# Performance work log

Hardware: AMD Instinct MI355X
Metric: run time of the kernel (lower is better)

The kernel has to match this reference:

```python
import jax, jax.numpy as jnp
import numpy as np

FEATURE_DIM = 512
NUM_HEADS = 8
HEAD_DIM = FEATURE_DIM // NUM_HEADS
B, L = 4, 2048


def setup_inputs() -> dict:
    key = jax.random.key(0)
    ks = jax.random.split(key, 10)
    s = 1.0 / np.sqrt(FEATURE_DIM)
    inp = {
        "ppg": jax.random.normal(ks[0], (B, FEATURE_DIM, L), dtype=jnp.float32),
        "ecg": jax.random.normal(ks[1], (B, FEATURE_DIM, L), dtype=jnp.float32),
        "Wq": jax.random.uniform(ks[2], (FEATURE_DIM, FEATURE_DIM), jnp.float32, -s, s),
        "bq": jnp.zeros((FEATURE_DIM,), jnp.float32),
        "Wk": jax.random.uniform(ks[3], (FEATURE_DIM, FEATURE_DIM), jnp.float32, -s, s),
        "bk": jnp.zeros((FEATURE_DIM,), jnp.float32),
        "Wv": jax.random.uniform(ks[4], (FEATURE_DIM, FEATURE_DIM), jnp.float32, -s, s),
        "bv": jnp.zeros((FEATURE_DIM,), jnp.float32),
        "Wo": jax.random.uniform(ks[5], (FEATURE_DIM, FEATURE_DIM), jnp.float32, -s, s),
        "bo": jnp.zeros((FEATURE_DIM,), jnp.float32),
    }
    return inp


def reference(ppg, ecg, Wq, bq, Wk, bk, Wv, bv, Wo, bo):
    # ppg/ecg: (B, C, L) -> (B, L, C)
    x = jnp.transpose(ppg, (0, 2, 1))
    y = jnp.transpose(ecg, (0, 2, 1))
    q = x @ Wq.T + bq  # (B, L, C)
    k = y @ Wk.T + bk
    v = y @ Wv.T + bv
    # split heads: (B, H, L, D)
    def split(t):
        return jnp.transpose(t.reshape(B, L, NUM_HEADS, HEAD_DIM), (0, 2, 1, 3))
    qh, kh, vh = split(q), split(k), split(v)
    scores = jnp.einsum('bhqd,bhkd->bhqk', qh, kh) / jnp.sqrt(jnp.float32(HEAD_DIM))
    probs = jax.nn.softmax(scores, axis=-1)  # dropout is identity in eval mode
    ctx = jnp.einsum('bhqk,bhkd->bhqd', probs, vh)
    ctx = jnp.transpose(ctx, (0, 2, 1, 3)).reshape(B, L, FEATURE_DIM)
    out = ctx @ Wo.T + bo + x  # residual with transposed ppg
    return jnp.transpose(out, (0, 2, 1))  # (B, C, L)
```

## Files before the change

### kernel.cpp

```cpp
#include <hip/hip_runtime.h>
#include <hip/hip_bf16.h>

static constexpr int Bc = 4;
static constexpr int Lc = 2048;
static constexpr int Cc = 512;
static constexpr int Hc = 8;
static constexpr int Dc = 64;

using short8  = __attribute__((ext_vector_type(8))) short;
using float4v = __attribute__((ext_vector_type(4))) float;

static __device__ __forceinline__ unsigned short f2bf(float f) {
    __hip_bfloat16 h = __float2bfloat16(f);
    return *reinterpret_cast<unsigned short*>(&h);
}

__global__ __launch_bounds__(256) void prep_kernel(
    const float* __restrict__ ppg, const float* __restrict__ ecg,
    const float* __restrict__ Wq, const float* __restrict__ Wk,
    const float* __restrict__ Wv, const float* __restrict__ Wo,
    unsigned short* __restrict__ Xt_ppg, unsigned short* __restrict__ Xt_ecg,
    unsigned short* __restrict__ Wbf)
{
    __shared__ float Ts[64 * 69];
    const int task = blockIdx.x;
    const int tid  = threadIdx.x;

    if (task < 2048) {
        const int src = task >> 10;
        const int rem = task & 1023;
        const int b   = rem >> 8;
        const int c0  = ((rem >> 5) & 7) * 64;
        const int l0  = (rem & 31) * 64;
        const float* X = src ? ecg : ppg;
        unsigned short* Xt = src ? Xt_ecg : Xt_ppg;

        #pragma unroll
        for (int j = 0; j < 4; ++j) {
            int idx = tid + j * 256;
            int c = idx >> 4, l4 = idx & 15;
            float4 v = *(const float4*)(X + ((size_t)b * Cc + c0 + c) * Lc + l0 + l4 * 4);
            Ts[c * 69 + l4 * 4 + 0] = v.x;
            Ts[c * 69 + l4 * 4 + 1] = v.y;
            Ts[c * 69 + l4 * 4 + 2] = v.z;
            Ts[c * 69 + l4 * 4 + 3] = v.w;
        }
        __syncthreads();
        #pragma unroll
        for (int j = 0; j < 8; ++j) {
            int u = tid + j * 256;
            int l = u >> 5, p2 = u & 31;
            float a = Ts[(2 * p2) * 69 + l];
            float bb = Ts[(2 * p2 + 1) * 69 + l];
            ushort2 pk; pk.x = f2bf(a); pk.y = f2bf(bb);
            *(ushort2*)(Xt + ((size_t)b * Lc + l0 + l) * Cc + c0 + 2 * p2) = pk;
        }
    } else {
        const int wb   = task - 2048;
        const int widx = wb >> 7;
        const float* W = widx == 0 ? Wq : widx == 1 ? Wk : widx == 2 ? Wv : Wo;
        size_t off = (size_t)(wb & 127) * 2048 + (size_t)tid * 8;
        float4 v0 = *(const float4*)(W + off);
        float4 v1 = *(const float4*)(W + off + 4);
        unsigned short pk[8] = {f2bf(v0.x), f2bf(v0.y), f2bf(v0.z), f2bf(v0.w),
                                f2bf(v1.x), f2bf(v1.y), f2bf(v1.z), f2bf(v1.w)};
        *(short8*)(Wbf + (size_t)widx * Cc * Cc + off) = *(const short8*)pk;
    }
}

__global__ __launch_bounds__(256) void proj_kernel(
    const unsigned short* __restrict__ Xt_ppg,
    const unsigned short* __restrict__ Xt_ecg,
    const unsigned short* __restrict__ Wbf,
    const float* __restrict__ bq, const float* __restrict__ bk,
    const float* __restrict__ bv,
    unsigned short* __restrict__ Qw, unsigned short* __restrict__ Kw,
    unsigned short* __restrict__ Vtw)
{
    constexpr int LDW = 72;
    const int z = blockIdx.z, p = z >> 2, b = z & 3;
    const int l0 = blockIdx.x * 128, n0 = blockIdx.y * 128;
    const unsigned short* X = (p == 0) ? Xt_ppg : Xt_ecg;
    const unsigned short* W = Wbf + (size_t)p * Cc * Cc;
    const float* bias = (p == 0) ? bq : (p == 1) ? bk : bv;

    const int tid = threadIdx.x, wave = tid >> 6, lane = tid & 63;
    const int l16 = lane & 15, quad = lane >> 4;
    const int wr = wave >> 1, wc = wave & 1;

    __shared__ __align__(16) unsigned short At[128 * LDW];
    __shared__ __align__(16) unsigned short Bt[128 * LDW];

    float4v acc[4][4] = {};
    short8 areg[4], breg[4];

    const int srow = tid >> 3, sc8 = tid & 7;
    #pragma unroll
    for (int j = 0; j < 4; ++j) {
        areg[j] = *(const short8*)(X + ((size_t)b * Lc + l0 + srow + j * 32) * Cc + sc8 * 8);
        breg[j] = *(const short8*)(W + (size_t)(n0 + srow + j * 32) * Cc + sc8 * 8);
    }

    for (int c0 = 0; c0 < Cc; c0 += 64) {
        #pragma unroll
        for (int j = 0; j < 4; ++j) {
            *(short8*)&At[(srow + j * 32) * LDW + sc8 * 8] = areg[j];
            *(short8*)&Bt[(srow + j * 32) * LDW + sc8 * 8] = breg[j];
        }
        __syncthreads();

        if (c0 + 64 < Cc) {
            #pragma unroll
            for (int j = 0; j < 4; ++j) {
                areg[j] = *(const short8*)(X + ((size_t)b * Lc + l0 + srow + j * 32) * Cc
                                           + c0 + 64 + sc8 * 8);
                breg[j] = *(const short8*)(W + (size_t)(n0 + srow + j * 32) * Cc
                                           + c0 + 64 + sc8 * 8);
            }
        }

        const unsigned short* Am = (p < 2) ? At : Bt;
        const unsigned short* Bm = (p < 2) ? Bt : At;

        #pragma unroll
        for (int ks = 0; ks < 2; ++ks) {
            short8 bf[4];
            #pragma unroll
            for (int nt = 0; nt < 4; ++nt)
                bf[nt] = *(const short8*)&Bm[(wc * 64 + nt * 16 + l16) * LDW
                                             + ks * 32 + quad * 8];
            #pragma unroll
            for (int mt = 0; mt < 4; ++mt) {
                short8 af = *(const short8*)&Am[(wr * 64 + mt * 16 + l16) * LDW
                                                + ks * 32 + quad * 8];
                #pragma unroll
                for (int nt = 0; nt < 4; ++nt)
                    acc[mt][nt] = __builtin_amdgcn_mfma_f32_16x16x32_bf16(
                        af, bf[nt], acc[mt][nt], 0, 0, 0);
            }
        }
        __syncthreads();
    }

    if (p < 2) {
        const float sc = (p == 0) ? 0.18033688011112042f : 1.0f;
        unsigned short* dst = (p == 0) ? Qw : Kw;
        #pragma unroll
        for (int nt = 0; nt < 4; ++nt) {
            int n = n0 + wc * 64 + nt * 16 + l16;
            int h = n >> 6, d = n & 63;
            int bh = b * Hc + h;
            float bia = bias[n];
            #pragma unroll
            for (int mt = 0; mt < 4; ++mt) {
                #pragma unroll
                for (int r = 0; r < 4; ++r) {
                    int l = l0 + wr * 64 + mt * 16 + quad * 4 + r;
                    dst[((size_t)bh * Lc + l) * Dc + d] =
                        f2bf((acc[mt][nt][r] + bia) * sc);
                }
            }
        }
    } else {
        #pragma unroll
        for (int mt = 0; mt < 4; ++mt) {
            #pragma unroll
            for (int r = 0; r < 4; ++r) {
                int n = n0 + wr * 64 + mt * 16 + quad * 4 + r;
                int h = n >> 6, d = n & 63;
                int bh = b * Hc + h;
                float bia = bias[n];
                #pragma unroll
                for (int nt = 0; nt < 4; ++nt) {
                    int l = l0 + wc * 64 + nt * 16 + l16;
                    Vtw[((size_t)bh * Dc + d) * Lc + l] = f2bf(acc[mt][nt][r] + bia);
                }
            }
        }
    }
}

__global__ __launch_bounds__(256, 4) void attn_mfma_kernel(
    const unsigned short* __restrict__ Qg,
    const unsigned short* __restrict__ Kg,
    const unsigned short* __restrict__ Vtg,
    float* __restrict__ O0, float* __restrict__ O1,
    float* __restrict__ lpart)
{
    constexpr int LDW = 72;
    const int bh    = blockIdx.y;
    const int split = blockIdx.z;
    const int q0    = blockIdx.x * 128;
    const int tid   = threadIdx.x;
    const int wave  = tid >> 6;
    const int lane  = tid & 63;
    const int l16   = lane & 15;
    const int quad  = lane >> 4;

    __shared__ __align__(16) unsigned short Kt[64 * LDW];
    __shared__ __align__(16) unsigned short Vt[64 * LDW];
    __shared__ __align__(16) unsigned short PT[128 * LDW];

    const int srow = tid >> 3, sc8 = tid & 7;

    const unsigned short* Qb = Qg + ((size_t)bh * Lc + q0) * Dc;
    #pragma unroll
    for (int j = 0; j < 4; ++j)
        *(short8*)&PT[(srow + j * 32) * LDW + sc8 * 8] =
            *(const short8*)(Qb + (srow + j * 32) * Dc + sc8 * 8);
    __syncthreads();

    short8 qf[2][2];
    #pragma unroll
    for (int qt = 0; qt < 2; ++qt)
        #pragma unroll
        for (int ks = 0; ks < 2; ++ks)
            qf[qt][ks] = *(const short8*)&PT[(wave * 32 + qt * 16 + l16) * LDW
                                             + ks * 32 + quad * 8];

    float4v O[2][4] = {};
    float lsum[2] = {0.0f, 0.0f};

    const unsigned short* Kb0 = Kg + (size_t)bh * Lc * Dc;
    const unsigned short* Vb0 = Vtg + (size_t)bh * (Dc * Lc);
    const int kbase = split * (Lc / 2);

    short8 kreg[2], vreg[2];
    #pragma unroll
    for (int j = 0; j < 2; ++j) {
        kreg[j] = *(const short8*)(Kb0 + (size_t)(kbase + srow + j * 32) * Dc + sc8 * 8);
        vreg[j] = *(const short8*)(Vb0 + (size_t)(srow + j * 32) * Lc + kbase + sc8 * 8);
    }

    for (int kc = kbase; kc < kbase + Lc / 2; kc += 64) {
        #pragma unroll
        for (int j = 0; j < 2; ++j) {
            *(short8*)&Kt[(srow + j * 32) * LDW + sc8 * 8] = kreg[j];
            *(short8*)&Vt[(srow + j * 32) * LDW + sc8 * 8] = vreg[j];
        }
        __syncthreads();

        if (kc + 64 < kbase + Lc / 2) {
            #pragma unroll
            for (int j = 0; j < 2; ++j) {
                kreg[j] = *(const short8*)(Kb0 + (size_t)(kc + 64 + srow + j * 32) * Dc
                                           + sc8 * 8);
                vreg[j] = *(const short8*)(Vb0 + (size_t)(srow + j * 32) * Lc
                                           + kc + 64 + sc8 * 8);
            }
        }

        float4v S[4][2];
        #pragma unroll
        for (int kt = 0; kt < 4; ++kt)
            #pragma unroll
            for (int qt = 0; qt < 2; ++qt)
                S[kt][qt] = (float4v){0.f, 0.f, 0.f, 0.f};
        #pragma unroll
        for (int ks = 0; ks < 2; ++ks) {
            #pragma unroll
            for (int kt = 0; kt < 4; ++kt) {
                short8 af = *(const short8*)&Kt[(kt * 16 + l16) * LDW
                                                + ks * 32 + quad * 8];
                #pragma unroll
                for (int qt = 0; qt < 2; ++qt)
                    S[kt][qt] = __builtin_amdgcn_mfma_f32_16x16x32_bf16(
                        af, qf[qt][ks], S[kt][qt], 0, 0, 0);
            }
        }

        #pragma unroll
        for (int qt = 0; qt < 2; ++qt) {
            #pragma unroll
            for (int kt = 0; kt < 4; ++kt) {
                float p0 = __builtin_amdgcn_exp2f(S[kt][qt][0]);
                float p1 = __builtin_amdgcn_exp2f(S[kt][qt][1]);
                float p2 = __builtin_amdgcn_exp2f(S[kt][qt][2]);
                float p3 = __builtin_amdgcn_exp2f(S[kt][qt][3]);
                lsum[qt] += (p0 + p1) + (p2 + p3);
                ushort4 pk;
                pk.x = f2bf(p0); pk.y = f2bf(p1); pk.z = f2bf(p2); pk.w = f2bf(p3);
                *(ushort4*)&PT[(wave * 32 + qt * 16 + l16) * LDW
                               + kt * 16 + quad * 4] = pk;
            }
        }

        #pragma unroll
        for (int ks = 0; ks < 2; ++ks) {
            short8 pf[2];
            #pragma unroll
            for (int qt = 0; qt < 2; ++qt)
                pf[qt] = *(const short8*)&PT[(wave * 32 + qt * 16 + l16) * LDW
                                             + ks * 32 + quad * 8];
            #pragma unroll
            for (int dt = 0; dt < 4; ++dt) {
                short8 vf = *(const short8*)&Vt[(dt * 16 + l16) * LDW
                                                + ks * 32 + quad * 8];
                #pragma unroll
                for (int qt = 0; qt < 2; ++qt)
                    O[qt][dt] = __builtin_amdgcn_mfma_f32_16x16x32_bf16(
                        pf[qt], vf, O[qt][dt], 0, 0, 0);
            }
        }
        __syncthreads();
    }

    const int b = bh >> 3, h = bh & 7;
    float* Op = split ? O1 : O0;
    float* lp = lpart + (size_t)split * (Bc * Hc) * Lc + (size_t)bh * Lc;

    #pragma unroll
    for (int qt = 0; qt < 2; ++qt) {
        float t = lsum[qt];
        t += __shfl_xor(t, 16, 64);
        t += __shfl_xor(t, 32, 64);
        if (quad == 0)
            lp[q0 + wave * 32 + qt * 16 + l16] = t;
        #pragma unroll
        for (int dt = 0; dt < 4; ++dt) {
            #pragma unroll
            for (int r = 0; r < 4; ++r) {
                int q = q0 + wave * 32 + qt * 16 + quad * 4 + r;
                Op[((size_t)b * Lc + q) * Cc + h * Dc + dt * 16 + l16] =
                    O[qt][dt][r];
            }
        }
    }
}

__global__ __launch_bounds__(256) void combine_kernel(
    const float* __restrict__ O0, const float* __restrict__ O1,
    const float* __restrict__ lpart, unsigned short* __restrict__ ctx)
{
    const int row = blockIdx.x;
    const int b   = row >> 11;
    const int l   = row & (Lc - 1);
    const int tid = threadIdx.x;
    const int c   = tid * 2;
    const int h   = c >> 6;

    const size_t lplane = (size_t)(Bc * Hc) * Lc;
    float denom = lpart[(size_t)(b * Hc + h) * Lc + l]
                + lpart[lplane + (size_t)(b * Hc + h) * Lc + l];
    float inv = 1.0f / denom;

    size_t off = (size_t)row * Cc + c;
    float2 a = *(const float2*)(O0 + off);
    float2 bb = *(const float2*)(O1 + off);
    ushort2 pk;
    pk.x = f2bf((a.x + bb.x) * inv);
    pk.y = f2bf((a.y + bb.y) * inv);
    *(ushort2*)(ctx + off) = pk;
}

__global__ __launch_bounds__(256) void outproj_kernel(
    const unsigned short* __restrict__ ctx, const unsigned short* __restrict__ Wo_bf,
    const float* __restrict__ bo, const float* __restrict__ ppg,
    float* __restrict__ out)
{
    constexpr int LDW = 72;
    const int b = blockIdx.z;
    const int l0 = blockIdx.x * 128, n0 = blockIdx.y * 64;
    const int tid = threadIdx.x, wave = tid >> 6, lane = tid & 63;
    const int l16 = lane & 15, quad = lane >> 4;

    __shared__ __align__(16) unsigned short At[64 * LDW];
    __shared__ __align__(16) unsigned short Bt[128 * LDW];

    float4v acc[4][2] = {};
    short8 areg[2], breg[4];

    const int srow = tid >> 3, sc8 = tid & 7;
    #pragma unroll
    for (int j = 0; j < 2; ++j)
        areg[j] = *(const short8*)(Wo_bf + (size_t)(n0 + srow + j * 32) * Cc + sc8 * 8);
    #pragma unroll
    for (int j = 0; j < 4; ++j)
        breg[j] = *(const short8*)(ctx + ((size_t)b * Lc + l0 + srow + j * 32) * Cc + sc8 * 8);

    for (int c0 = 0; c0 < Cc; c0 += 64) {
        #pragma unroll
        for (int j = 0; j < 2; ++j)
            *(short8*)&At[(srow + j * 32) * LDW + sc8 * 8] = areg[j];
        #pragma unroll
        for (int j = 0; j < 4; ++j)
            *(short8*)&Bt[(srow + j * 32) * LDW + sc8 * 8] = breg[j];
        __syncthreads();

        if (c0 + 64 < Cc) {
            #pragma unroll
            for (int j = 0; j < 2; ++j)
                areg[j] = *(const short8*)(Wo_bf + (size_t)(n0 + srow + j * 32) * Cc
                                           + c0 + 64 + sc8 * 8);
            #pragma unroll
            for (int j = 0; j < 4; ++j)
                breg[j] = *(const short8*)(ctx + ((size_t)b * Lc + l0 + srow + j * 32) * Cc
                                           + c0 + 64 + sc8 * 8);
        }

        #pragma unroll
        for (int ks = 0; ks < 2; ++ks) {
            short8 bf[2];
            #pragma unroll
            for (int nt = 0; nt < 2; ++nt)
                bf[nt] = *(const short8*)&Bt[(wave * 32 + nt * 16 + l16) * LDW
                                             + ks * 32 + quad * 8];
            #pragma unroll
            for (int mt = 0; mt < 4; ++mt) {
                short8 af = *(const short8*)&At[(mt * 16 + l16) * LDW
                                                + ks * 32 + quad * 8];
                #pragma unroll
                for (int nt = 0; nt < 2; ++nt)
                    acc[mt][nt] = __builtin_amdgcn_mfma_f32_16x16x32_bf16(
                        af, bf[nt], acc[mt][nt], 0, 0, 0);
            }
        }
        __syncthreads();
    }

    #pragma unroll
    for (int mt = 0; mt < 4; ++mt) {
        #pragma unroll
        for (int r = 0; r < 4; ++r) {
            int n = n0 + mt * 16 + quad * 4 + r;
            float bia = bo[n];
            #pragma unroll
            for (int nt = 0; nt < 2; ++nt) {
                int l = l0 + wave * 32 + nt * 16 + l16;
                size_t oidx = ((size_t)b * Cc + n) * Lc + l;
                out[oidx] = acc[mt][nt][r] + bia + ppg[oidx];
            }
        }
    }
}

extern "C" void kernel_launch(void* const* d_in, const int* in_sizes, int n_in,
                              void* d_out, int out_size, void* d_ws, size_t ws_size,
                              hipStream_t stream) {
    const float* ppg = (const float*)d_in[0];
    const float* ecg = (const float*)d_in[1];
    const float* Wq  = (const float*)d_in[2];
    const float* bq  = (const float*)d_in[3];
    const float* Wk  = (const float*)d_in[4];
    const float* bk  = (const float*)d_in[5];
    const float* Wv  = (const float*)d_in[6];
    const float* bv  = (const float*)d_in[7];
    const float* Wo  = (const float*)d_in[8];
    const float* bo  = (const float*)d_in[9];
    float* out = (float*)d_out;

    unsigned short* base   = (unsigned short*)d_ws;
    const size_t M = 1024 * 1024;
    unsigned short* Xt_ppg = base;
    unsigned short* Xt_ecg = base + 4 * M;
    unsigned short* Wbf    = base + 8 * M;
    unsigned short* Qw     = base + 9 * M;
    unsigned short* Kw     = base + 13 * M;
    unsigned short* Vtw    = base + 17 * M;
    float* Opart0 = (float*)base;
    float* Opart1 = (float*)(base + 21 * M);
    float* lpart  = (float*)(base + 29 * M);
    unsigned short* ctx = Qw;

    prep_kernel<<<2560, 256, 0, stream>>>(ppg, ecg, Wq, Wk, Wv, Wo,
                                          Xt_ppg, Xt_ecg, Wbf);

    dim3 g1(Lc / 128, Cc / 128, 3 * Bc);
    proj_kernel<<<g1, 256, 0, stream>>>(Xt_ppg, Xt_ecg, Wbf, bq, bk, bv,
                                        Qw, Kw, Vtw);

    dim3 g2(Lc / 128, Bc * Hc, 2);
    attn_mfma_kernel<<<g2, 256, 0, stream>>>(Qw, Kw, Vtw, Opart0, Opart1, lpart);

    combine_kernel<<<Bc * Lc, 256, 0, stream>>>(Opart0, Opart1, lpart, ctx);

    dim3 g3(Lc / 128, Cc / 64, Bc);
    outproj_kernel<<<g3, 256, 0, stream>>>(ctx, Wbf + (size_t)3 * Cc * Cc,
                                           bo, ppg, out);
}
```

Before: 184.7 us.

## Fuse split-K combine into attention via atomic counter, enlarge attention and outproj tiles

Removes the separate combine kernel: each attention block writes its partial output in bf16, bumps a per-tile atomic counter, and the second-arriving block reads the other partial plus both row sums to write the normalized ctx. The attention tile grows to 256 queries per block, which doubles K/V reuse at the cost of registers (launch bounds drop to 2 blocks per SM). The output projection tile grows to 128x128 with a 2x2 wave layout. This adds a memset, threadfences and bf16 rounding of the partial sums, and halves the attention grid to 256 blocks, which may underfill the device.

```diff
diff --git a/kernel.cpp b/kernel.cpp
--- a/kernel.cpp
+++ b/kernel.cpp
@@ -13,6 +13,9 @@
 static __device__ __forceinline__ unsigned short f2bf(float f) {
     __hip_bfloat16 h = __float2bfloat16(f);
     return *reinterpret_cast<unsigned short*>(&h);
+}
+static __device__ __forceinline__ float bf2f(unsigned short u) {
+    return __uint_as_float(((unsigned int)u) << 16);
 }
 
 __global__ __launch_bounds__(256) void prep_kernel(
@@ -180,17 +183,20 @@
     }
 }
 
-__global__ __launch_bounds__(256, 4) void attn_mfma_kernel(
+__global__ __launch_bounds__(256, 2) void attn_mfma_kernel(
     const unsigned short* __restrict__ Qg,
     const unsigned short* __restrict__ Kg,
     const unsigned short* __restrict__ Vtg,
-    float* __restrict__ O0, float* __restrict__ O1,
-    float* __restrict__ lpart)
+    unsigned short* __restrict__ Opart0,
+    unsigned short* __restrict__ Opart1,
+    float* __restrict__ lpart,
+    unsigned short* __restrict__ ctx,
+    int* __restrict__ ctr)
 {
     constexpr int LDW = 72;
     const int bh    = blockIdx.y;
     const int split = blockIdx.z;
-    const int q0    = blockIdx.x * 128;
+    const int q0    = blockIdx.x * 256;
     const int tid   = threadIdx.x;
     const int wave  = tid >> 6;
     const int lane  = tid & 63;
@@ -199,27 +205,28 @@
 
     __shared__ __align__(16) unsigned short Kt[64 * LDW];
     __shared__ __align__(16) unsigned short Vt[64 * LDW];
-    __shared__ __align__(16) unsigned short PT[128 * LDW];
+    __shared__ __align__(16) unsigned short PT[256 * LDW];
+    __shared__ int s_old;
 
     const int srow = tid >> 3, sc8 = tid & 7;
 
     const unsigned short* Qb = Qg + ((size_t)bh * Lc + q0) * Dc;
     #pragma unroll
-    for (int j = 0; j < 4; ++j)
+    for (int j = 0; j < 8; ++j)
         *(short8*)&PT[(srow + j * 32) * LDW + sc8 * 8] =
             *(const short8*)(Qb + (srow + j * 32) * Dc + sc8 * 8);
     __syncthreads();
 
-    short8 qf[2][2];
-    #pragma unroll
-    for (int qt = 0; qt < 2; ++qt)
+    short8 qf[4][2];
+    #pragma unroll
+    for (int qt = 0; qt < 4; ++qt)
         #pragma unroll
         for (int ks = 0; ks < 2; ++ks)
-            qf[qt][ks] = *(const short8*)&PT[(wave * 32 + qt * 16 + l16) * LDW
+            qf[qt][ks] = *(const short8*)&PT[(wave * 64 + qt * 16 + l16) * LDW
                                              + ks * 32 + quad * 8];
 
-    float4v O[2][4] = {};
-    float lsum[2] = {0.0f, 0.0f};
+    float4v O[4][4] = {};
+    float lsum[4] = {0.f, 0.f, 0.f, 0.f};
 
     const unsigned short* Kb0 = Kg + (size_t)bh * Lc * Dc;
     const unsigned short* Vb0 = Vtg + (size_t)bh * (Dc * Lc);
@@ -250,11 +257,11 @@
             }
         }
 
-        float4v S[4][2];
+        float4v S[4][4];
         #pragma unroll
         for (int kt = 0; kt < 4; ++kt)
             #pragma unroll
-            for (int qt = 0; qt < 2; ++qt)
+            for (int qt = 0; qt < 4; ++qt)
                 S[kt][qt] = (float4v){0.f, 0.f, 0.f, 0.f};
         #pragma unroll
         for (int ks = 0; ks < 2; ++ks) {
@@ -263,14 +270,14 @@
                 short8 af = *(const short8*)&Kt[(kt * 16 + l16) * LDW
                                                 + ks * 32 + quad * 8];
                 #pragma unroll
-                for (int qt = 0; qt < 2; ++qt)
+                for (int qt = 0; qt < 4; ++qt)
                     S[kt][qt] = __builtin_amdgcn_mfma_f32_16x16x32_bf16(
                         af, qf[qt][ks], S[kt][qt], 0, 0, 0);
             }
         }
 
         #pragma unroll
-        for (int qt = 0; qt < 2; ++qt) {
+        for (int qt = 0; qt < 4; ++qt) {
             #pragma unroll
             for (int kt = 0; kt < 4; ++kt) {
                 float p0 = __builtin_amdgcn_exp2f(S[kt][qt][0]);
@@ -280,24 +287,24 @@
                 lsum[qt] += (p0 + p1) + (p2 + p3);
                 ushort4 pk;
                 pk.x = f2bf(p0); pk.y = f2bf(p1); pk.z = f2bf(p2); pk.w = f2bf(p3);
-                *(ushort4*)&PT[(wave * 32 + qt * 16 + l16) * LDW
+                *(ushort4*)&PT[(wave * 64 + qt * 16 + l16) * LDW
                                + kt * 16 + quad * 4] = pk;
             }
         }
 
         #pragma unroll
         for (int ks = 0; ks < 2; ++ks) {
-            short8 pf[2];
-            #pragma unroll
-            for (int qt = 0; qt < 2; ++qt)
-                pf[qt] = *(const short8*)&PT[(wave * 32 + qt * 16 + l16) * LDW
+            short8 pf[4];
+            #pragma unroll
+            for (int qt = 0; qt < 4; ++qt)
+                pf[qt] = *(const short8*)&PT[(wave * 64 + qt * 16 + l16) * LDW
                                              + ks * 32 + quad * 8];
             #pragma unroll
             for (int dt = 0; dt < 4; ++dt) {
                 short8 vf = *(const short8*)&Vt[(dt * 16 + l16) * LDW
                                                 + ks * 32 + quad * 8];
                 #pragma unroll
-                for (int qt = 0; qt < 2; ++qt)
+                for (int qt = 0; qt < 4; ++qt)
                     O[qt][dt] = __builtin_amdgcn_mfma_f32_16x16x32_bf16(
                         pf[qt], vf, O[qt][dt], 0, 0, 0);
             }
@@ -306,51 +313,56 @@
     }
 
     const int b = bh >> 3, h = bh & 7;
-    float* Op = split ? O1 : O0;
+    unsigned short* Om = split ? Opart1 : Opart0;
     float* lp = lpart + (size_t)split * (Bc * Hc) * Lc + (size_t)bh * Lc;
 
     #pragma unroll
-    for (int qt = 0; qt < 2; ++qt) {
+    for (int qt = 0; qt < 4; ++qt) {
         float t = lsum[qt];
         t += __shfl_xor(t, 16, 64);
         t += __shfl_xor(t, 32, 64);
         if (quad == 0)
-            lp[q0 + wave * 32 + qt * 16 + l16] = t;
+            lp[q0 + wave * 64 + qt * 16 + l16] = t;
+    }
+    #pragma unroll
+    for (int qt = 0; qt < 4; ++qt) {
         #pragma unroll
         for (int dt = 0; dt < 4; ++dt) {
             #pragma unroll
             for (int r = 0; r < 4; ++r) {
-                int q = q0 + wave * 32 + qt * 16 + quad * 4 + r;
-                Op[((size_t)b * Lc + q) * Cc + h * Dc + dt * 16 + l16] =
-                    O[qt][dt][r];
-            }
-        }
-    }
-}
-
-__global__ __launch_bounds__(256) void combine_kernel(
-    const float* __restrict__ O0, const float* __restrict__ O1,
-    const float* __restrict__ lpart, unsigned short* __restrict__ ctx)
-{
-    const int row = blockIdx.x;
-    const int b   = row >> 11;
-    const int l   = row & (Lc - 1);
-    const int tid = threadIdx.x;
-    const int c   = tid * 2;
-    const int h   = c >> 6;
-
-    const size_t lplane = (size_t)(Bc * Hc) * Lc;
-    float denom = lpart[(size_t)(b * Hc + h) * Lc + l]
-                + lpart[lplane + (size_t)(b * Hc + h) * Lc + l];
-    float inv = 1.0f / denom;
-
-    size_t off = (size_t)row * Cc + c;
-    float2 a = *(const float2*)(O0 + off);
-    float2 bb = *(const float2*)(O1 + off);
-    ushort2 pk;
-    pk.x = f2bf((a.x + bb.x) * inv);
-    pk.y = f2bf((a.y + bb.y) * inv);
-    *(ushort2*)(ctx + off) = pk;
+                int q = q0 + wave * 64 + qt * 16 + quad * 4 + r;
+                Om[((size_t)b * Lc + q) * Cc + h * Dc + dt * 16 + l16] =
+                    f2bf(O[qt][dt][r]);
+            }
+        }
+    }
+
+    __threadfence();
+    __syncthreads();
+    if (tid == 0)
+        s_old = atomicAdd(&ctr[bh * 8 + blockIdx.x], 1);
+    __syncthreads();
+
+    if (s_old == 1) {
+        __threadfence();
+        const unsigned short* Oo = split ? Opart0 : Opart1;
+        const float* lp0 = lpart + (size_t)bh * Lc;
+        const float* lp1 = lpart + (size_t)(Bc * Hc) * Lc + (size_t)bh * Lc;
+        #pragma unroll
+        for (int qt = 0; qt < 4; ++qt) {
+            #pragma unroll
+            for (int r = 0; r < 4; ++r) {
+                int q = q0 + wave * 64 + qt * 16 + quad * 4 + r;
+                float inv = 1.0f / (lp0[q] + lp1[q]);
+                #pragma unroll
+                for (int dt = 0; dt < 4; ++dt) {
+                    size_t off = ((size_t)b * Lc + q) * Cc + h * Dc + dt * 16 + l16;
+                    float other = bf2f(Oo[off]);
+                    ctx[off] = f2bf((O[qt][dt][r] + other) * inv);
+                }
+            }
+        }
+    }
 }
 
 __global__ __launch_bounds__(256) void outproj_kernel(
@@ -360,57 +372,55 @@
 {
     constexpr int LDW = 72;
     const int b = blockIdx.z;
-    const int l0 = blockIdx.x * 128, n0 = blockIdx.y * 64;
+    const int l0 = blockIdx.x * 128, n0 = blockIdx.y * 128;
     const int tid = threadIdx.x, wave = tid >> 6, lane = tid & 63;
     const int l16 = lane & 15, quad = lane >> 4;
-
-    __shared__ __align__(16) unsigned short At[64 * LDW];
+    const int wr = wave >> 1, wc = wave & 1;
+
+    __shared__ __align__(16) unsigned short At[128 * LDW];
     __shared__ __align__(16) unsigned short Bt[128 * LDW];
 
-    float4v acc[4][2] = {};
-    short8 areg[2], breg[4];
+    float4v acc[4][4] = {};
+    short8 areg[4], breg[4];
 
     const int srow = tid >> 3, sc8 = tid & 7;
     #pragma unroll
-    for (int j = 0; j < 2; ++j)
+    for (int j = 0; j < 4; ++j) {
         areg[j] = *(const short8*)(Wo_bf + (size_t)(n0 + srow + j * 32) * Cc + sc8 * 8);
-    #pragma unroll
-    for (int j = 0; j < 4; ++j)
         breg[j] = *(const short8*)(ctx + ((size_t)b * Lc + l0 + srow + j * 32) * Cc + sc8 * 8);
+    }
 
     for (int c0 = 0; c0 < Cc; c0 += 64) {
         #pragma unroll
-        for (int j = 0; j < 2; ++j)
+        for (int j = 0; j < 4; ++j) {
             *(short8*)&At[(srow + j * 32) * LDW + sc8 * 8] = areg[j];
-        #pragma unroll
-        for (int j = 0; j < 4; ++j)
             *(short8*)&Bt[(srow + j * 32) * LDW + sc8 * 8] = breg[j];
+        }
         __syncthreads();
 
         if (c0 + 64 < Cc) {
             #pragma unroll
-            for (int j = 0; j < 2; ++j)
+            for (int j = 0; j < 4; ++j) {
                 areg[j] = *(const short8*)(Wo_bf + (size_t)(n0 + srow + j * 32) * Cc
                                            + c0 + 64 + sc8 * 8);
-            #pragma unroll
-            for (int j = 0; j < 4; ++j)
                 breg[j] = *(const short8*)(ctx + ((size_t)b * Lc + l0 + srow + j * 32) * Cc
                                            + c0 + 64 + sc8 * 8);
+            }
         }
 
         #pragma unroll
         for (int ks = 0; ks < 2; ++ks) {
-            short8 bf[2];
-            #pragma unroll
-            for (int nt = 0; nt < 2; ++nt)
-                bf[nt] = *(const short8*)&Bt[(wave * 32 + nt * 16 + l16) * LDW
+            short8 bf[4];
+            #pragma unroll
+            for (int nt = 0; nt < 4; ++nt)
+                bf[nt] = *(const short8*)&Bt[(wc * 64 + nt * 16 + l16) * LDW
                                              + ks * 32 + quad * 8];
             #pragma unroll
             for (int mt = 0; mt < 4; ++mt) {
-                short8 af = *(const short8*)&At[(mt * 16 + l16) * LDW
+                short8 af = *(const short8*)&At[(wr * 64 + mt * 16 + l16) * LDW
                                                 + ks * 32 + quad * 8];
                 #pragma unroll
-                for (int nt = 0; nt < 2; ++nt)
+                for (int nt = 0; nt < 4; ++nt)
                     acc[mt][nt] = __builtin_amdgcn_mfma_f32_16x16x32_bf16(
                         af, bf[nt], acc[mt][nt], 0, 0, 0);
             }
@@ -422,11 +432,11 @@
     for (int mt = 0; mt < 4; ++mt) {
         #pragma unroll
         for (int r = 0; r < 4; ++r) {
-            int n = n0 + mt * 16 + quad * 4 + r;
+            int n = n0 + wr * 64 + mt * 16 + quad * 4 + r;
             float bia = bo[n];
             #pragma unroll
-            for (int nt = 0; nt < 2; ++nt) {
-                int l = l0 + wave * 32 + nt * 16 + l16;
+            for (int nt = 0; nt < 4; ++nt) {
+                int l = l0 + wc * 64 + nt * 16 + l16;
                 size_t oidx = ((size_t)b * Cc + n) * Lc + l;
                 out[oidx] = acc[mt][nt][r] + bia + ppg[oidx];
             }
@@ -457,10 +467,13 @@
     unsigned short* Qw     = base + 9 * M;
     unsigned short* Kw     = base + 13 * M;
     unsigned short* Vtw    = base + 17 * M;
-    float* Opart0 = (float*)base;
-    float* Opart1 = (float*)(base + 21 * M);
-    float* lpart  = (float*)(base + 29 * M);
-    unsigned short* ctx = Qw;
+    unsigned short* ctx    = base + 21 * M;
+    float* lpart = (float*)(base + 25 * M);
+    int*   ctr   = (int*)(base + 25 * M + 262144);
+    unsigned short* Opart0 = base;
+    unsigned short* Opart1 = base + 4 * M;
+
+    hipMemsetAsync(ctr, 0, 32 * 8 * sizeof(int), stream);
 
     prep_kernel<<<2560, 256, 0, stream>>>(ppg, ecg, Wq, Wk, Wv, Wo,
                                           Xt_ppg, Xt_ecg, Wbf);
@@ -469,12 +482,11 @@
     proj_kernel<<<g1, 256, 0, stream>>>(Xt_ppg, Xt_ecg, Wbf, bq, bk, bv,
                                         Qw, Kw, Vtw);
 
-    dim3 g2(Lc / 128, Bc * Hc, 2);
-    attn_mfma_kernel<<<g2, 256, 0, stream>>>(Qw, Kw, Vtw, Opart0, Opart1, lpart);
-
-    combine_kernel<<<Bc * Lc, 256, 0, stream>>>(Opart0, Opart1, lpart, ctx);
-
-    dim3 g3(Lc / 128, Cc / 64, Bc);
+    dim3 g2(Lc / 256, Bc * Hc, 2);
+    attn_mfma_kernel<<<g2, 256, 0, stream>>>(Qw, Kw, Vtw, Opart0, Opart1,
+                                             lpart, ctx, ctr);
+
+    dim3 g3(Lc / 128, Cc / 128, Bc);
     outproj_kernel<<<g3, 256, 0, stream>>>(ctx, Wbf + (size_t)3 * Cc * Cc,
                                            bo, ppg, out);
 }
```

Measured after the change: 291.0 us. 57.5% more time.

## Fuse split-K attention combine into output projection with bf16 partials

Applied to the files above, without the earlier changes.

The attention kernel now writes its two split partial outputs as bf16 instead of fp32, and the separate combine kernel is removed. The output projection reads both partials and the row sums, normalizes and converts to bf16 while staging its tiles in shared memory. The output tile grows to 128x128 per block. This removes one launch and the fp32 partial round trip, but drops the register prefetch double-buffering in the out-projection, redoes the combine work once per n-block, and adds rounding error from the bf16 partials.

```diff
diff --git a/kernel.cpp b/kernel.cpp
--- a/kernel.cpp
+++ b/kernel.cpp
@@ -13,6 +13,9 @@
 static __device__ __forceinline__ unsigned short f2bf(float f) {
     __hip_bfloat16 h = __float2bfloat16(f);
     return *reinterpret_cast<unsigned short*>(&h);
+}
+static __device__ __forceinline__ float bf2f(unsigned short u) {
+    return __uint_as_float(((unsigned int)u) << 16);
 }
 
 __global__ __launch_bounds__(256) void prep_kernel(
@@ -184,7 +187,8 @@
     const unsigned short* __restrict__ Qg,
     const unsigned short* __restrict__ Kg,
     const unsigned short* __restrict__ Vtg,
-    float* __restrict__ O0, float* __restrict__ O1,
+    unsigned short* __restrict__ O0,
+    unsigned short* __restrict__ O1,
     float* __restrict__ lpart)
 {
     constexpr int LDW = 72;
@@ -306,7 +310,7 @@
     }
 
     const int b = bh >> 3, h = bh & 7;
-    float* Op = split ? O1 : O0;
+    unsigned short* Om = split ? O1 : O0;
     float* lp = lpart + (size_t)split * (Bc * Hc) * Lc + (size_t)bh * Lc;
 
     #pragma unroll
@@ -321,98 +325,75 @@
             #pragma unroll
             for (int r = 0; r < 4; ++r) {
                 int q = q0 + wave * 32 + qt * 16 + quad * 4 + r;
-                Op[((size_t)b * Lc + q) * Cc + h * Dc + dt * 16 + l16] =
-                    O[qt][dt][r];
-            }
-        }
-    }
-}
-
-__global__ __launch_bounds__(256) void combine_kernel(
-    const float* __restrict__ O0, const float* __restrict__ O1,
-    const float* __restrict__ lpart, unsigned short* __restrict__ ctx)
-{
-    const int row = blockIdx.x;
-    const int b   = row >> 11;
-    const int l   = row & (Lc - 1);
-    const int tid = threadIdx.x;
-    const int c   = tid * 2;
-    const int h   = c >> 6;
-
-    const size_t lplane = (size_t)(Bc * Hc) * Lc;
-    float denom = lpart[(size_t)(b * Hc + h) * Lc + l]
-                + lpart[lplane + (size_t)(b * Hc + h) * Lc + l];
-    float inv = 1.0f / denom;
-
-    size_t off = (size_t)row * Cc + c;
-    float2 a = *(const float2*)(O0 + off);
-    float2 bb = *(const float2*)(O1 + off);
-    ushort2 pk;
-    pk.x = f2bf((a.x + bb.x) * inv);
-    pk.y = f2bf((a.y + bb.y) * inv);
-    *(ushort2*)(ctx + off) = pk;
+                Om[((size_t)b * Lc + q) * Cc + h * Dc + dt * 16 + l16] =
+                    f2bf(O[qt][dt][r]);
+            }
+        }
+    }
 }
 
 __global__ __launch_bounds__(256) void outproj_kernel(
-    const unsigned short* __restrict__ ctx, const unsigned short* __restrict__ Wo_bf,
+    const unsigned short* __restrict__ O0, const unsigned short* __restrict__ O1,
+    const float* __restrict__ lpart,
+    const unsigned short* __restrict__ Wo_bf,
     const float* __restrict__ bo, const float* __restrict__ ppg,
     float* __restrict__ out)
 {
     constexpr int LDW = 72;
     const int b = blockIdx.z;
-    const int l0 = blockIdx.x * 128, n0 = blockIdx.y * 64;
+    const int l0 = blockIdx.x * 128, n0 = blockIdx.y * 128;
     const int tid = threadIdx.x, wave = tid >> 6, lane = tid & 63;
     const int l16 = lane & 15, quad = lane >> 4;
-
-    __shared__ __align__(16) unsigned short At[64 * LDW];
+    const int wr = wave >> 1, wc = wave & 1;
+
+    __shared__ __align__(16) unsigned short At[128 * LDW];
     __shared__ __align__(16) unsigned short Bt[128 * LDW];
 
-    float4v acc[4][2] = {};
-    short8 areg[2], breg[4];
-
+    float4v acc[4][4] = {};
     const int srow = tid >> 3, sc8 = tid & 7;
-    #pragma unroll
-    for (int j = 0; j < 2; ++j)
-        areg[j] = *(const short8*)(Wo_bf + (size_t)(n0 + srow + j * 32) * Cc + sc8 * 8);
-    #pragma unroll
-    for (int j = 0; j < 4; ++j)
-        breg[j] = *(const short8*)(ctx + ((size_t)b * Lc + l0 + srow + j * 32) * Cc + sc8 * 8);
+    const size_t lplane = (size_t)(Bc * Hc) * Lc;
 
     for (int c0 = 0; c0 < Cc; c0 += 64) {
-        #pragma unroll
-        for (int j = 0; j < 2; ++j)
-            *(short8*)&At[(srow + j * 32) * LDW + sc8 * 8] = areg[j];
-        #pragma unroll
-        for (int j = 0; j < 4; ++j)
-            *(short8*)&Bt[(srow + j * 32) * LDW + sc8 * 8] = breg[j];
-        __syncthreads();
-
-        if (c0 + 64 < Cc) {
-            #pragma unroll
-            for (int j = 0; j < 2; ++j)
-                areg[j] = *(const short8*)(Wo_bf + (size_t)(n0 + srow + j * 32) * Cc
-                                           + c0 + 64 + sc8 * 8);
-            #pragma unroll
-            for (int j = 0; j < 4; ++j)
-                breg[j] = *(const short8*)(ctx + ((size_t)b * Lc + l0 + srow + j * 32) * Cc
-                                           + c0 + 64 + sc8 * 8);
-        }
+        const int h = c0 >> 6;
+        const float* lp0 = lpart + (size_t)(b * Hc + h) * Lc;
+        const float* lp1 = lp0 + lplane;
+
+        #pragma unroll
+        for (int j = 0; j < 4; ++j) {
+            int row = srow + j * 32;
+            *(short8*)&At[row * LDW + sc8 * 8] =
+                *(const short8*)(Wo_bf + (size_t)(n0 + row) * Cc + c0 + sc8 * 8);
+            int l = l0 + row;
+            float inv = 1.0f / (lp0[l] + lp1[l]);
+            size_t off = ((size_t)b * Lc + l) * Cc + c0 + sc8 * 8;
+            short8 a8 = *(const short8*)(O0 + off);
+            short8 b8 = *(const short8*)(O1 + off);
+            unsigned short pk[8];
+            #pragma unroll
+            for (int e = 0; e < 8; ++e) {
+                unsigned short ua = ((const unsigned short*)&a8)[e];
+                unsigned short ub = ((const unsigned short*)&b8)[e];
+                pk[e] = f2bf((bf2f(ua) + bf2f(ub)) * inv);
+            }
+            *(short8*)&Bt[row * LDW + sc8 * 8] = *(const short8*)pk;
+        }
+        __syncthreads();
 
         #pragma unroll
         for (int ks = 0; ks < 2; ++ks) {
-            short8 bf[2];
-            #pragma unroll
-            for (int nt = 0; nt < 2; ++nt)
-                bf[nt] = *(const short8*)&Bt[(wave * 32 + nt * 16 + l16) * LDW
-                                             + ks * 32 + quad * 8];
+            short8 bfr[4];
+            #pragma unroll
+            for (int nt = 0; nt < 4; ++nt)
+                bfr[nt] = *(const short8*)&Bt[(wc * 64 + nt * 16 + l16) * LDW
+                                              + ks * 32 + quad * 8];
             #pragma unroll
             for (int mt = 0; mt < 4; ++mt) {
-                short8 af = *(const short8*)&At[(mt * 16 + l16) * LDW
+                short8 af = *(const short8*)&At[(wr * 64 + mt * 16 + l16) * LDW
                                                 + ks * 32 + quad * 8];
                 #pragma unroll
-                for (int nt = 0; nt < 2; ++nt)
+                for (int nt = 0; nt < 4; ++nt)
                     acc[mt][nt] = __builtin_amdgcn_mfma_f32_16x16x32_bf16(
-                        af, bf[nt], acc[mt][nt], 0, 0, 0);
+                        af, bfr[nt], acc[mt][nt], 0, 0, 0);
             }
         }
         __syncthreads();
@@ -422,11 +403,11 @@
     for (int mt = 0; mt < 4; ++mt) {
         #pragma unroll
         for (int r = 0; r < 4; ++r) {
-            int n = n0 + mt * 16 + quad * 4 + r;
+            int n = n0 + wr * 64 + mt * 16 + quad * 4 + r;
             float bia = bo[n];
             #pragma unroll
-            for (int nt = 0; nt < 2; ++nt) {
-                int l = l0 + wave * 32 + nt * 16 + l16;
+            for (int nt = 0; nt < 4; ++nt) {
+                int l = l0 + wc * 64 + nt * 16 + l16;
                 size_t oidx = ((size_t)b * Cc + n) * Lc + l;
                 out[oidx] = acc[mt][nt][r] + bia + ppg[oidx];
             }
@@ -457,10 +438,9 @@
     unsigned short* Qw     = base + 9 * M;
     unsigned short* Kw     = base + 13 * M;
     unsigned short* Vtw    = base + 17 * M;
-    float* Opart0 = (float*)base;
-    float* Opart1 = (float*)(base + 21 * M);
-    float* lpart  = (float*)(base + 29 * M);
-    unsigned short* ctx = Qw;
+    float* lpart = (float*)(base + 21 * M);
+    unsigned short* Opart0 = base;
+    unsigned short* Opart1 = base + 4 * M;
 
     prep_kernel<<<2560, 256, 0, stream>>>(ppg, ecg, Wq, Wk, Wv, Wo,
                                           Xt_ppg, Xt_ecg, Wbf);
@@ -472,9 +452,8 @@
     dim3 g2(Lc / 128, Bc * Hc, 2);
     attn_mfma_kernel<<<g2, 256, 0, stream>>>(Qw, Kw, Vtw, Opart0, Opart1, lpart);
 
-    combine_kernel<<<Bc * Lc, 256, 0, stream>>>(Opart0, Opart1, lpart, ctx);
-
-    dim3 g3(Lc / 128, Cc / 64, Bc);
-    outproj_kernel<<<g3, 256, 0, stream>>>(ctx, Wbf + (size_t)3 * Cc * Cc,
+    dim3 g3(Lc / 128, Cc / 128, Bc);
+    outproj_kernel<<<g3, 256, 0, stream>>>(Opart0, Opart1, lpart,
+                                           Wbf + (size_t)3 * Cc * Cc,
                                            bo, ppg, out);
 }
```

After: 184.0 us. About the same (-0.4%).
